# Optimization experiments

Hardware: AMD Instinct MI355X
Metric: run time of the kernel (lower is better)

## Reference

```python
import jax, jax.numpy as jnp
import numpy as np

SCALING = 2.0  # lora alpha / r

def setup_inputs() -> dict:
    key = jax.random.key(0)
    k1, k2, k3, k4, k5 = jax.random.split(key, 5)
    B, S, D_IN, D_OUT, R = 4, 2048, 4096, 4096, 16
    x = jax.random.normal(k1, (B, S, D_IN), dtype=jnp.float32)
    weight = jax.random.normal(k2, (D_OUT, D_IN), dtype=jnp.float32) * 0.02
    lora_A = jax.random.normal(k3, (R, D_IN), dtype=jnp.float32) * (1.0 / np.sqrt(D_IN))
    lora_B = jax.random.normal(k4, (D_OUT, R), dtype=jnp.float32) * 0.02
    bias = jax.random.normal(k5, (D_OUT,), dtype=jnp.float32) * 0.02
    return {"x": x, "weight": weight, "lora_A": lora_A, "lora_B": lora_B, "bias": bias}

def reference(x, weight, lora_A, lora_B, bias):
    # Faithful to the torch module: materialize W + scaling * (B @ A), then F.linear.
    # effective_weight: [d_out, d_in]
    effective_weight = weight + SCALING * (lora_B @ lora_A)
    # F.linear(x, W, b) = x @ W.T + b
    out = jnp.einsum('bsd,od->bso', x, effective_weight) + bias
    return out
```

## Files before the change

kernel.cpp:

```cpp
#include <hip/hip_runtime.h>
#include <hip/hip_bf16.h>
#include <stdint.h>

typedef unsigned short u16;
typedef u16 u16x4 __attribute__((ext_vector_type(4)));
typedef short bf16x8 __attribute__((ext_vector_type(8)));
typedef float f32x4 __attribute__((ext_vector_type(4)));

__device__ __forceinline__ u16 f2bf(float f) {
  union { float f; uint32_t u; } v; v.f = f;
  uint32_t u = v.u;
  return (u16)((u + 0x7fffu + ((u >> 16) & 1u)) >> 16);
}

__global__ __launch_bounds__(256) void aux_kernel(
    const float4* __restrict__ x, u16x4* __restrict__ xb, int n4, int nCvt,
    const float* __restrict__ W, const float* __restrict__ A,
    const float* __restrict__ Bl, u16* __restrict__ Wout, int DIN) {
  if ((int)blockIdx.x < nCvt) {
    int i = blockIdx.x * 256 + threadIdx.x;
    const int stride = nCvt * 256;
    for (; i < n4; i += stride) {
      float4 v = x[i];
      u16x4 o;
      o.x = f2bf(v.x); o.y = f2bf(v.y); o.z = f2bf(v.z); o.w = f2bf(v.w);
      xb[i] = o;
    }
  } else {
    const int n = blockIdx.x - nCvt;
    float bv[16];
#pragma unroll
    for (int r = 0; r < 16; ++r) bv[r] = 2.0f * Bl[n * 16 + r];
    const int iters = DIN / (256 * 4);
    for (int c = 0; c < iters; ++c) {
      const int k = (c * 256 + (int)threadIdx.x) * 4;
      float4 wv = *(const float4*)&W[(size_t)n * DIN + k];
#pragma unroll
      for (int r = 0; r < 16; ++r) {
        const float4 av = *(const float4*)&A[(size_t)r * DIN + k];
        wv.x += bv[r] * av.x;
        wv.y += bv[r] * av.y;
        wv.z += bv[r] * av.z;
        wv.w += bv[r] * av.w;
      }
      u16x4 o;
      o.x = f2bf(wv.x); o.y = f2bf(wv.y); o.z = f2bf(wv.z); o.w = f2bf(wv.w);
      *(u16x4*)&Wout[(size_t)n * DIN + k] = o;
    }
  }
}

#define BM 256
#define BN 128

__global__ __launch_bounds__(512, 4) void gemm_kernel(
    const u16* __restrict__ A, const u16* __restrict__ B,
    const float* __restrict__ bias, float* __restrict__ C,
    int M, int N, int K) {
  extern __shared__ u16 lds[];

  const int tid  = threadIdx.x;
  const int lane = tid & 63;
  const int wid  = tid >> 6;

  const int nwg = gridDim.x;
  const int cpx = nwg >> 3;
  const int f   = ((int)blockIdx.x & 7) * cpx + ((int)blockIdx.x >> 3);
  const int nbx = N / BN;
  const int bx = f % nbx, by = f / nbx;
  const int bm = by * BM, bn = bx * BN;

  const int wm = (wid >> 1) * 64;
  const int wn = (wid & 1) * 64;
  const int lr = lane & 15;
  const int lk = lane >> 4;
  const int rslot = ((lk ^ ((lr >> 1) & 3)) << 3);

  const int srow  = tid >> 2;
  const int sslot = (((tid & 3) ^ ((tid >> 3) & 3)) << 3);
  const u16* gA = A + (size_t)(bm + srow) * K + sslot;
  const u16* gB = B + (size_t)(bn + srow) * K + sslot;

  auto stage = [&](int sb , int kt ) {
    const u16* sa = gA + (size_t)kt * 32;
#pragma unroll
    for (int i = 0; i < 2; ++i)
      __builtin_amdgcn_global_load_lds(
          (__attribute__((address_space(1))) const void*)(sa + (size_t)i * 128 * K),
          (__attribute__((address_space(3))) void*)(&lds[sb + wid * 512 + i * 4096]),
          16, 0, 0);
    __builtin_amdgcn_global_load_lds(
        (__attribute__((address_space(1))) const void*)(gB + (size_t)kt * 32),
        (__attribute__((address_space(3))) void*)(&lds[sb + 8192 + wid * 512]),
        16, 0, 0);
  };

  f32x4 acc[4][4];
#pragma unroll
  for (int i = 0; i < 4; ++i)
#pragma unroll
    for (int n = 0; n < 4; ++n) acc[i][n] = f32x4{0.f, 0.f, 0.f, 0.f};

  const int NS = K >> 5;
  int sb0 = 0, sb1 = 12288, sb2 = 24576;
  stage(sb0, 0);
  stage(sb1, 1);

  for (int s = 0; s < NS; ++s) {
    asm volatile("s_waitcnt vmcnt(3)" ::: "memory");
    __builtin_amdgcn_s_barrier();
    const int kt = (s + 2 < NS) ? s + 2 : 0;
    stage(sb2, kt);

    bf16x8 b[4], a[4];
#pragma unroll
    for (int n = 0; n < 4; ++n)
      b[n] = *(const bf16x8*)&lds[sb0 + 8192 + (wn + n * 16 + lr) * 32 + rslot];
#pragma unroll
    for (int m = 0; m < 4; ++m)
      a[m] = *(const bf16x8*)&lds[sb0 + (wm + m * 16 + lr) * 32 + rslot];

#pragma unroll
    for (int m = 0; m < 4; ++m)
#pragma unroll
      for (int n = 0; n < 4; ++n)
        acc[m][n] = __builtin_amdgcn_mfma_f32_16x16x32_bf16(a[m], b[n], acc[m][n], 0, 0, 0);

    const int t = sb0; sb0 = sb1; sb1 = sb2; sb2 = t;
  }

  asm volatile("s_waitcnt vmcnt(0)" ::: "memory");
  __builtin_amdgcn_s_barrier();

#pragma unroll
  for (int nf = 0; nf < 4; ++nf) {
    const int col = bn + wn + nf * 16 + lr;
    const float bv = bias[col];
#pragma unroll
    for (int mf = 0; mf < 4; ++mf) {
      const int row = bm + wm + mf * 16 + lk * 4;
#pragma unroll
      for (int j = 0; j < 4; ++j)
        C[(size_t)(row + j) * N + col] = acc[mf][nf][j] + bv;
    }
  }
}

extern "C" void kernel_launch(void* const* d_in, const int* in_sizes, int n_in,
                              void* d_out, int out_size, void* d_ws, size_t ws_size,
                              hipStream_t stream) {
  const float* x  = (const float*)d_in[0];
  const float* w  = (const float*)d_in[1];
  const float* lA = (const float*)d_in[2];
  const float* lB = (const float*)d_in[3];
  const float* bs = (const float*)d_in[4];
  float* out = (float*)d_out;

  const int DOUT = in_sizes[4];
  const int DIN  = in_sizes[1] / DOUT;
  const int M    = in_sizes[0] / DIN;

  u16* Xb = (u16*)d_ws;
  u16* Wb = Xb + (size_t)M * DIN;

  const int n4 = (M * DIN) / 4;
  const int nCvt = 2048;
  aux_kernel<<<nCvt + DOUT, 256, 0, stream>>>((const float4*)x, (u16x4*)Xb, n4, nCvt,
                                              w, lA, lB, Wb, DIN);

  (void)hipFuncSetAttribute((const void*)gemm_kernel,
                            hipFuncAttributeMaxDynamicSharedMemorySize, 73728);

  const int nwg = (M / BM) * (DOUT / BN);
  gemm_kernel<<<nwg, 512, 73728, stream>>>(Xb, Wb, bs, out, M, DOUT, DIN);
}
```

Measured before the change: 375.8 us.

## Pre-swizzle weight into MFMA fragment layout and load B directly to registers

The aux kernel now writes the merged LoRA weight in bf16, laid out per MFMA fragment (16 columns by 32 k per 512-element block), so each GEMM lane can load its B fragment straight from global memory into registers. B no longer goes through LDS. The GEMM tile grows to 256x256, with each wave computing 128x64 and double-buffered B registers. LDS drops to A only, and MFMA issue gets raised priority. The aim is to cut LDS traffic and raise reuse per tile, at the cost of more accumulator registers (occupancy bound falls to 2) and exposed global-load latency for B.

```diff
diff --git a/kernel.cpp b/kernel.cpp
--- a/kernel.cpp
+++ b/kernel.cpp
@@ -4,6 +4,7 @@
 
 typedef unsigned short u16;
 typedef u16 u16x4 __attribute__((ext_vector_type(4)));
+typedef u16 u16x8 __attribute__((ext_vector_type(8)));
 typedef short bf16x8 __attribute__((ext_vector_type(8)));
 typedef float f32x4 __attribute__((ext_vector_type(4)));
 
@@ -16,7 +17,7 @@
 __global__ __launch_bounds__(256) void aux_kernel(
     const float4* __restrict__ x, u16x4* __restrict__ xb, int n4, int nCvt,
     const float* __restrict__ W, const float* __restrict__ A,
-    const float* __restrict__ Bl, u16* __restrict__ Wout, int DIN) {
+    const float* __restrict__ Bl, u16* __restrict__ Wf, int DIN) {
   if ((int)blockIdx.x < nCvt) {
     int i = blockIdx.x * 256 + threadIdx.x;
     const int stride = nCvt * 256;
@@ -27,34 +28,37 @@
       xb[i] = o;
     }
   } else {
-    const int n = blockIdx.x - nCvt;
-    float bv[16];
+    const int bb  = (int)blockIdx.x - nCvt;
+    const int tid = threadIdx.x;
+    const int w   = tid >> 6, l = tid & 63;
+    const int KS  = DIN >> 5;
+    const int fid = bb * 4 + w;
+    const int nf  = fid / KS, ks = fid % KS;
+    const int col = nf * 16 + (l & 15);
+    const int kb  = ks * 32 + ((l >> 4) << 3);
+
+    float4 s0 = *(const float4*)&W[(size_t)col * DIN + kb];
+    float4 s1 = *(const float4*)&W[(size_t)col * DIN + kb + 4];
 #pragma unroll
-    for (int r = 0; r < 16; ++r) bv[r] = 2.0f * Bl[n * 16 + r];
-    const int iters = DIN / (256 * 4);
-    for (int c = 0; c < iters; ++c) {
-      const int k = (c * 256 + (int)threadIdx.x) * 4;
-      float4 wv = *(const float4*)&W[(size_t)n * DIN + k];
-#pragma unroll
-      for (int r = 0; r < 16; ++r) {
-        const float4 av = *(const float4*)&A[(size_t)r * DIN + k];
-        wv.x += bv[r] * av.x;
-        wv.y += bv[r] * av.y;
-        wv.z += bv[r] * av.z;
-        wv.w += bv[r] * av.w;
-      }
-      u16x4 o;
-      o.x = f2bf(wv.x); o.y = f2bf(wv.y); o.z = f2bf(wv.z); o.w = f2bf(wv.w);
-      *(u16x4*)&Wout[(size_t)n * DIN + k] = o;
+    for (int r = 0; r < 16; ++r) {
+      const float bv = 2.0f * Bl[col * 16 + r];
+      const float4 a0 = *(const float4*)&A[(size_t)r * DIN + kb];
+      const float4 a1 = *(const float4*)&A[(size_t)r * DIN + kb + 4];
+      s0.x += bv * a0.x; s0.y += bv * a0.y; s0.z += bv * a0.z; s0.w += bv * a0.w;
+      s1.x += bv * a1.x; s1.y += bv * a1.y; s1.z += bv * a1.z; s1.w += bv * a1.w;
     }
+    u16x8 o;
+    o[0] = f2bf(s0.x); o[1] = f2bf(s0.y); o[2] = f2bf(s0.z); o[3] = f2bf(s0.w);
+    o[4] = f2bf(s1.x); o[5] = f2bf(s1.y); o[6] = f2bf(s1.z); o[7] = f2bf(s1.w);
+    *(u16x8*)&Wf[(size_t)fid * 512 + l * 8] = o;
   }
 }
 
 #define BM 256
-#define BN 128
+#define BN 256
 
-__global__ __launch_bounds__(512, 4) void gemm_kernel(
-    const u16* __restrict__ A, const u16* __restrict__ B,
+__global__ __launch_bounds__(512, 2) void gemm_kernel(
+    const u16* __restrict__ A, const u16* __restrict__ Bf,
     const float* __restrict__ bias, float* __restrict__ C,
     int M, int N, int K) {
   extern __shared__ u16 lds[];
@@ -70,75 +74,85 @@
   const int bx = f % nbx, by = f / nbx;
   const int bm = by * BM, bn = bx * BN;
 
-  const int wm = (wid >> 1) * 64;
-  const int wn = (wid & 1) * 64;
-  const int lr = lane & 15;
-  const int lk = lane >> 4;
+  const int wmL = (wid >> 2) * 128;
+  const int wnL = (wid & 3) * 64;
+  const int lr  = lane & 15;
+  const int lk  = lane >> 4;
   const int rslot = ((lk ^ ((lr >> 1) & 3)) << 3);
 
   const int srow  = tid >> 2;
   const int sslot = (((tid & 3) ^ ((tid >> 3) & 3)) << 3);
   const u16* gA = A + (size_t)(bm + srow) * K + sslot;
-  const u16* gB = B + (size_t)(bn + srow) * K + sslot;
 
-  auto stage = [&](int sb , int kt ) {
-    const u16* sa = gA + (size_t)kt * 32;
+  const int NS = K >> 5;
+  const int nfg0 = (bn + wnL) >> 4;
+
+  auto stageA = [&](int sb, int kt) {
+    const u16* s = gA + (size_t)kt * 32;
 #pragma unroll
     for (int i = 0; i < 2; ++i)
       __builtin_amdgcn_global_load_lds(
-          (__attribute__((address_space(1))) const void*)(sa + (size_t)i * 128 * K),
+          (__attribute__((address_space(1))) const void*)(s + (size_t)i * 128 * K),
           (__attribute__((address_space(3))) void*)(&lds[sb + wid * 512 + i * 4096]),
           16, 0, 0);
-    __builtin_amdgcn_global_load_lds(
-        (__attribute__((address_space(1))) const void*)(gB + (size_t)kt * 32),
-        (__attribute__((address_space(3))) void*)(&lds[sb + 8192 + wid * 512]),
-        16, 0, 0);
+  };
+  auto gfrag = [&](int nf, int s) -> bf16x8 {
+    return *(const bf16x8*)&Bf[((size_t)(nfg0 + nf) * NS + s) * 512 + (lane << 3)];
   };
 
-  f32x4 acc[4][4];
+  f32x4 acc[8][4];
 #pragma unroll
-  for (int i = 0; i < 4; ++i)
+  for (int i = 0; i < 8; ++i)
 #pragma unroll
     for (int n = 0; n < 4; ++n) acc[i][n] = f32x4{0.f, 0.f, 0.f, 0.f};
 
-  const int NS = K >> 5;
-  int sb0 = 0, sb1 = 12288, sb2 = 24576;
-  stage(sb0, 0);
-  stage(sb1, 1);
+  int sb0 = 0, sb1 = 8192, sb2 = 16384;
+  bf16x8 B0[4], B1[4];
 
-  for (int s = 0; s < NS; ++s) {
-    asm volatile("s_waitcnt vmcnt(3)" ::: "memory");
-    __builtin_amdgcn_s_barrier();
-    const int kt = (s + 2 < NS) ? s + 2 : 0;
-    stage(sb2, kt);
+  stageA(sb0, 0);
+  stageA(sb1, 1);
+#pragma unroll
+  for (int n = 0; n < 4; ++n) B0[n] = gfrag(n, 0);
 
-    bf16x8 b[4], a[4];
-#pragma unroll
-    for (int n = 0; n < 4; ++n)
-      b[n] = *(const bf16x8*)&lds[sb0 + 8192 + (wn + n * 16 + lr) * 32 + rslot];
-#pragma unroll
-    for (int m = 0; m < 4; ++m)
-      a[m] = *(const bf16x8*)&lds[sb0 + (wm + m * 16 + lr) * 32 + rslot];
+#define STEP(BC, BG, S)                                                        \
+  do {                                                                         \
+    asm volatile("s_waitcnt vmcnt(6)" ::: "memory");                           \
+    __builtin_amdgcn_s_barrier();                                              \
+    stageA(sb2, ((S) + 2 < NS) ? (S) + 2 : 0);                                 \
+    const int sg_ = ((S) + 1 < NS) ? (S) + 1 : 0;                              \
+    _Pragma("unroll")                                                          \
+    for (int n = 0; n < 4; ++n) BG[n] = gfrag(n, sg_);                         \
+    bf16x8 a_[8];                                                              \
+    _Pragma("unroll")                                                          \
+    for (int m = 0; m < 8; ++m)                                                \
+      a_[m] = *(const bf16x8*)&lds[sb0 + (wmL + m * 16 + lr) * 32 + rslot];    \
+    __builtin_amdgcn_s_setprio(1);                                             \
+    _Pragma("unroll")                                                          \
+    for (int m = 0; m < 8; ++m)                                                \
+      _Pragma("unroll")                                                        \
+      for (int n = 0; n < 4; ++n)                                              \
+        acc[m][n] = __builtin_amdgcn_mfma_f32_16x16x32_bf16(a_[m], BC[n],      \
+                                                            acc[m][n], 0, 0, 0); \
+    __builtin_amdgcn_s_setprio(0);                                             \
+    int t_ = sb0; sb0 = sb1; sb1 = sb2; sb2 = t_;                              \
+  } while (0)
 
-#pragma unroll
-    for (int m = 0; m < 4; ++m)
-#pragma unroll
-      for (int n = 0; n < 4; ++n)
-        acc[m][n] = __builtin_amdgcn_mfma_f32_16x16x32_bf16(a[m], b[n], acc[m][n], 0, 0, 0);
-
-    const int t = sb0; sb0 = sb1; sb1 = sb2; sb2 = t;
+  for (int it = 0; it < NS / 2; ++it) {
+    STEP(B0, B1, 2 * it);
+    STEP(B1, B0, 2 * it + 1);
   }
+#undef STEP
 
   asm volatile("s_waitcnt vmcnt(0)" ::: "memory");
   __builtin_amdgcn_s_barrier();
 
 #pragma unroll
   for (int nf = 0; nf < 4; ++nf) {
-    const int col = bn + wn + nf * 16 + lr;
+    const int col = bn + wnL + nf * 16 + lr;
     const float bv = bias[col];
 #pragma unroll
-    for (int mf = 0; mf < 4; ++mf) {
-      const int row = bm + wm + mf * 16 + lk * 4;
+    for (int mf = 0; mf < 8; ++mf) {
+      const int row = bm + wmL + mf * 16 + lk * 4;
 #pragma unroll
       for (int j = 0; j < 4; ++j)
         C[(size_t)(row + j) * N + col] = acc[mf][nf][j] + bv;
@@ -161,16 +175,17 @@
   const int M    = in_sizes[0] / DIN;
 
   u16* Xb = (u16*)d_ws;
-  u16* Wb = Xb + (size_t)M * DIN;
+  u16* Wf = Xb + (size_t)M * DIN;
 
   const int n4 = (M * DIN) / 4;
   const int nCvt = 2048;
-  aux_kernel<<<nCvt + DOUT, 256, 0, stream>>>((const float4*)x, (u16x4*)Xb, n4, nCvt,
-                                              w, lA, lB, Wb, DIN);
+  const int nW = (DOUT >> 4) * (DIN >> 5) / 4;
+  aux_kernel<<<nCvt + nW, 256, 0, stream>>>((const float4*)x, (u16x4*)Xb, n4, nCvt,
+                                            w, lA, lB, Wf, DIN);
 
   (void)hipFuncSetAttribute((const void*)gemm_kernel,
-                            hipFuncAttributeMaxDynamicSharedMemorySize, 73728);
+                            hipFuncAttributeMaxDynamicSharedMemorySize, 49152);
 
   const int nwg = (M / BM) * (DOUT / BN);
-  gemm_kernel<<<nwg, 512, 73728, stream>>>(Xb, Wb, bs, out, M, DOUT, DIN);
+  gemm_kernel<<<nwg, 512, 49152, stream>>>(Xb, Wf, bs, out, M, DOUT, DIN);
 }
```

New measurement: 373.6 us. No clear change (-0.6%).

## Enlarge GEMM tile to 256x256 with ping-pong LDS pipeline over K=64 steps

Applied to the files above, without the earlier changes.

Changes the bf16 GEMM tile from 256x128 to 256x256 with eight waves in a 2x4 layout, each holding 128x64 of accumulators. The main loop now stages K=64 per step into two LDS parity buffers, about 128KB in total. Global-to-LDS loads are interleaved between quarter-blocks of MFMAs, separated by barriers, with s_setprio raised around the MFMA bursts. The aim is higher arithmetic intensity per LDS byte and better overlap of loads with compute, at the cost of more registers, lower occupancy (launch bounds of 2), and many more barriers.

```diff
diff --git a/kernel.cpp b/kernel.cpp
--- a/kernel.cpp
+++ b/kernel.cpp
@@ -51,9 +51,9 @@
 }
 
 #define BM 256
-#define BN 128
-
-__global__ __launch_bounds__(512, 4) void gemm_kernel(
+#define BN 256
+
+__global__ __launch_bounds__(512, 2) void gemm_kernel(
     const u16* __restrict__ A, const u16* __restrict__ B,
     const float* __restrict__ bias, float* __restrict__ C,
     int M, int N, int K) {
@@ -70,63 +70,135 @@
   const int bx = f % nbx, by = f / nbx;
   const int bm = by * BM, bn = bx * BN;
 
-  const int wm = (wid >> 1) * 64;
-  const int wn = (wid & 1) * 64;
-  const int lr = lane & 15;
-  const int lk = lane >> 4;
-  const int rslot = ((lk ^ ((lr >> 1) & 3)) << 3);
-
-  const int srow  = tid >> 2;
-  const int sslot = (((tid & 3) ^ ((tid >> 3) & 3)) << 3);
-  const u16* gA = A + (size_t)(bm + srow) * K + sslot;
-  const u16* gB = B + (size_t)(bn + srow) * K + sslot;
-
-  auto stage = [&](int sb , int kt ) {
-    const u16* sa = gA + (size_t)kt * 32;
-#pragma unroll
-    for (int i = 0; i < 2; ++i)
-      __builtin_amdgcn_global_load_lds(
-          (__attribute__((address_space(1))) const void*)(sa + (size_t)i * 128 * K),
-          (__attribute__((address_space(3))) void*)(&lds[sb + wid * 512 + i * 4096]),
-          16, 0, 0);
-    __builtin_amdgcn_global_load_lds(
-        (__attribute__((address_space(1))) const void*)(gB + (size_t)kt * 32),
-        (__attribute__((address_space(3))) void*)(&lds[sb + 8192 + wid * 512]),
-        16, 0, 0);
+  const int wmL = (wid >> 2) * 128;
+  const int wnL = (wid & 3) * 64;
+  const int lr  = lane & 15;
+  const int lk  = lane >> 4;
+
+  u16* const avp = &lds[lane * 8 + ((wid >> 2) * 8) * 512];
+  u16* const bvp = &lds[32768 + lane * 8 + ((wid & 3) * 4) * 512];
+
+  auto ldA = [&](int par, int ks, int mf) -> bf16x8 {
+    return *(const bf16x8*)(avp + (par * 2 + ks) * 8192 + mf * 512);
   };
-
-  f32x4 acc[4][4];
-#pragma unroll
-  for (int i = 0; i < 4; ++i)
+  auto ldB = [&](int par, int ks, int nf) -> bf16x8 {
+    return *(const bf16x8*)(bvp + (par * 2 + ks) * 8192 + nf * 512);
+  };
+
+  const int skoff = lk << 3;
+  const u16* gA0 = A + (size_t)(bm + wid * 16 + lr) * K + skoff;
+  const u16* gA1 = A + (size_t)(bm + 128 + wid * 16 + lr) * K + skoff;
+  const u16* gB0 = B + (size_t)(bn + wid * 16 + lr) * K + skoff;
+  const u16* gB1 = B + (size_t)(bn + 128 + wid * 16 + lr) * K + skoff;
+
+#define STG(gsrc, opbase, par, half, kt)                                          \
+  do {                                                                            \
+    __builtin_amdgcn_global_load_lds(                                             \
+        (__attribute__((address_space(1))) const void*)((gsrc) + (size_t)(kt)*64),\
+        (__attribute__((address_space(3))) void*)(                                \
+            &lds[(opbase) + ((par)*2 + 0)*8192 + ((half)*8 + wid)*512]), 16, 0, 0);\
+    __builtin_amdgcn_global_load_lds(                                             \
+        (__attribute__((address_space(1))) const void*)((gsrc) + (size_t)(kt)*64 + 32),\
+        (__attribute__((address_space(3))) void*)(                                \
+            &lds[(opbase) + ((par)*2 + 1)*8192 + ((half)*8 + wid)*512]), 16, 0, 0);\
+  } while (0)
+#define STG_A(par, half, kt) STG((half) ? gA1 : gA0, 0, par, half, kt)
+#define STG_B(par, half, kt) STG((half) ? gB1 : gB0, 32768, par, half, kt)
+
+#define BAR()   __builtin_amdgcn_s_barrier()
+#define LGKM0() asm volatile("s_waitcnt lgkmcnt(0)" ::: "memory")
+#define LGKM8() asm volatile("s_waitcnt lgkmcnt(8)" ::: "memory")
+#define VM4()   asm volatile("s_waitcnt vmcnt(4)" ::: "memory")
+
+#define MFMA16(MB, NB, B0, B1)                                                    \
+  __builtin_amdgcn_s_setprio(1);                                                  \
+  _Pragma("unroll")                                                               \
+  for (int m = 0; m < 4; ++m)                                                     \
+    _Pragma("unroll")                                                             \
+    for (int n = 0; n < 2; ++n)                                                   \
+      acc[(MB) + m][(NB) + n] = __builtin_amdgcn_mfma_f32_16x16x32_bf16(          \
+          aA0[m], B0[n], acc[(MB) + m][(NB) + n], 0, 0, 0);                       \
+  _Pragma("unroll")                                                               \
+  for (int m = 0; m < 4; ++m)                                                     \
+    _Pragma("unroll")                                                             \
+    for (int n = 0; n < 2; ++n)                                                   \
+      acc[(MB) + m][(NB) + n] = __builtin_amdgcn_mfma_f32_16x16x32_bf16(          \
+          aA1[m], B1[n], acc[(MB) + m][(NB) + n], 0, 0, 0);                       \
+  __builtin_amdgcn_s_setprio(0)
+
+  f32x4 acc[8][4];
+#pragma unroll
+  for (int i = 0; i < 8; ++i)
 #pragma unroll
     for (int n = 0; n < 4; ++n) acc[i][n] = f32x4{0.f, 0.f, 0.f, 0.f};
 
-  const int NS = K >> 5;
-  int sb0 = 0, sb1 = 12288, sb2 = 24576;
-  stage(sb0, 0);
-  stage(sb1, 1);
-
-  for (int s = 0; s < NS; ++s) {
-    asm volatile("s_waitcnt vmcnt(3)" ::: "memory");
-    __builtin_amdgcn_s_barrier();
-    const int kt = (s + 2 < NS) ? s + 2 : 0;
-    stage(sb2, kt);
-
-    bf16x8 b[4], a[4];
-#pragma unroll
-    for (int n = 0; n < 4; ++n)
-      b[n] = *(const bf16x8*)&lds[sb0 + 8192 + (wn + n * 16 + lr) * 32 + rslot];
-#pragma unroll
-    for (int m = 0; m < 4; ++m)
-      a[m] = *(const bf16x8*)&lds[sb0 + (wm + m * 16 + lr) * 32 + rslot];
-
-#pragma unroll
-    for (int m = 0; m < 4; ++m)
-#pragma unroll
-      for (int n = 0; n < 4; ++n)
-        acc[m][n] = __builtin_amdgcn_mfma_f32_16x16x32_bf16(a[m], b[n], acc[m][n], 0, 0, 0);
-
-    const int t = sb0; sb0 = sb1; sb1 = sb2; sb2 = t;
+  const int NT = K >> 6;
+  STG_A(0, 0, 0); STG_A(0, 1, 0); STG_B(0, 0, 0); STG_B(0, 1, 0);
+  STG_B(1, 0, 1); STG_B(1, 1, 1);
+  VM4(); BAR();
+
+  bf16x8 aA0[4], aA1[4], b0_0[2], b0_1[2], b1_0[2], b1_1[2];
+
+  for (int i = 0; i < NT / 2; ++i) {
+    const int k1  = 2 * i + 1;
+    const int kt2 = (2 * i + 2 < NT) ? 2 * i + 2 : 0;
+    const int kt3 = (2 * i + 3 < NT) ? 2 * i + 3 : 0;
+
+#pragma unroll
+    for (int n = 0; n < 2; ++n) { b0_0[n] = ldB(0, 0, n); b0_1[n] = ldB(0, 1, n); }
+#pragma unroll
+    for (int m = 0; m < 4; ++m) { aA0[m] = ldA(0, 0, m); aA1[m] = ldA(0, 1, m); }
+    STG_A(1, 0, k1);
+    LGKM8(); BAR(); LGKM0();
+    MFMA16(0, 0, b0_0, b0_1);
+    BAR();
+
+#pragma unroll
+    for (int n = 0; n < 2; ++n) { b1_0[n] = ldB(0, 0, 2 + n); b1_1[n] = ldB(0, 1, 2 + n); }
+    STG_A(1, 1, k1);
+    BAR(); LGKM0();
+    MFMA16(0, 2, b1_0, b1_1);
+    BAR();
+
+#pragma unroll
+    for (int m = 0; m < 4; ++m) { aA0[m] = ldA(0, 0, 4 + m); aA1[m] = ldA(0, 1, 4 + m); }
+    STG_B(0, 0, kt2);
+    BAR(); LGKM0();
+    MFMA16(4, 0, b0_0, b0_1);
+    BAR();
+
+    STG_B(0, 1, kt2);
+    BAR(); LGKM0();
+    MFMA16(4, 2, b1_0, b1_1);
+    VM4(); BAR();
+
+#pragma unroll
+    for (int n = 0; n < 2; ++n) { b0_0[n] = ldB(1, 0, n); b0_1[n] = ldB(1, 1, n); }
+#pragma unroll
+    for (int m = 0; m < 4; ++m) { aA0[m] = ldA(1, 0, m); aA1[m] = ldA(1, 1, m); }
+    STG_A(0, 0, kt2);
+    LGKM8(); BAR(); LGKM0();
+    MFMA16(0, 0, b0_0, b0_1);
+    BAR();
+
+#pragma unroll
+    for (int n = 0; n < 2; ++n) { b1_0[n] = ldB(1, 0, 2 + n); b1_1[n] = ldB(1, 1, 2 + n); }
+    STG_A(0, 1, kt2);
+    BAR(); LGKM0();
+    MFMA16(0, 2, b1_0, b1_1);
+    BAR();
+
+#pragma unroll
+    for (int m = 0; m < 4; ++m) { aA0[m] = ldA(1, 0, 4 + m); aA1[m] = ldA(1, 1, 4 + m); }
+    STG_B(1, 0, kt3);
+    BAR(); LGKM0();
+    MFMA16(4, 0, b0_0, b0_1);
+    BAR();
+
+    STG_B(1, 1, kt3);
+    BAR(); LGKM0();
+    MFMA16(4, 2, b1_0, b1_1);
+    VM4(); BAR();
   }
 
   asm volatile("s_waitcnt vmcnt(0)" ::: "memory");
@@ -134,16 +206,24 @@
 
 #pragma unroll
   for (int nf = 0; nf < 4; ++nf) {
-    const int col = bn + wn + nf * 16 + lr;
+    const int col = bn + wnL + nf * 16 + lr;
     const float bv = bias[col];
 #pragma unroll
-    for (int mf = 0; mf < 4; ++mf) {
-      const int row = bm + wm + mf * 16 + lk * 4;
+    for (int mf = 0; mf < 8; ++mf) {
+      const int row = bm + wmL + mf * 16 + lk * 4;
 #pragma unroll
       for (int j = 0; j < 4; ++j)
         C[(size_t)(row + j) * N + col] = acc[mf][nf][j] + bv;
     }
   }
+#undef STG
+#undef STG_A
+#undef STG_B
+#undef BAR
+#undef LGKM0
+#undef LGKM8
+#undef VM4
+#undef MFMA16
 }
 
 extern "C" void kernel_launch(void* const* d_in, const int* in_sizes, int n_in,
@@ -169,8 +249,8 @@
                                               w, lA, lB, Wb, DIN);
 
   (void)hipFuncSetAttribute((const void*)gemm_kernel,
-                            hipFuncAttributeMaxDynamicSharedMemorySize, 73728);
+                            hipFuncAttributeMaxDynamicSharedMemorySize, 131072);
 
   const int nwg = (M / BM) * (DOUT / BN);
-  gemm_kernel<<<nwg, 512, 73728, stream>>>(Xb, Wb, bs, out, M, DOUT, DIN);
-}
+  gemm_kernel<<<nwg, 512, 131072, stream>>>(Xb, Wb, bs, out, M, DOUT, DIN);
+}
```

After: 363.8 us. -3.2%, faster.
